# Optimization experiments

Hardware: AMD Instinct MI355X
Metric: run time of the kernel (lower is better)

## Reference

```python
import jax, jax.numpy as jnp
import numpy as np

N_NODES = 100000
N_EDGES = 3200000
IN_CH = 256
OUT_CH = 1


def setup_inputs() -> dict:
    key = jax.random.key(0)
    ks = jax.random.split(key, 8)
    x = jax.random.normal(ks[0], (N_NODES, IN_CH), dtype=jnp.float32)
    edge_index = jax.random.randint(ks[1], (2, N_EDGES), 0, N_NODES, dtype=jnp.int64 if jax.config.jax_enable_x64 else jnp.int32)
    s_in = 1.0 / np.sqrt(IN_CH)
    Wq = jax.random.uniform(ks[2], (IN_CH, OUT_CH), jnp.float32, -s_in, s_in)
    bq = jax.random.uniform(ks[3], (OUT_CH,), jnp.float32, -s_in, s_in)
    Wk = jax.random.uniform(ks[4], (IN_CH, OUT_CH), jnp.float32, -s_in, s_in)
    bk = jax.random.uniform(ks[5], (OUT_CH,), jnp.float32, -s_in, s_in)
    Wv = jax.random.uniform(ks[6], (IN_CH, IN_CH), jnp.float32, -s_in, s_in)
    bv = jax.random.uniform(ks[7], (IN_CH,), jnp.float32, -s_in, s_in)
    return {"x": x, "edge_index": edge_index, "Wq": Wq, "bq": bq,
            "Wk": Wk, "bk": bk, "Wv": Wv, "bv": bv}


def reference(x, edge_index, Wq, bq, Wk, bk, Wv, bv):
    num_nodes = x.shape[0]
    q = x @ Wq + bq                       # [N, out_ch]
    k = x @ Wk + bk                       # [N, out_ch]
    v = x @ Wv + bv                       # [N, in_ch]
    row, col = edge_index[0], edge_index[1]
    # edge attention logits: gather + dot over out_ch
    att = jnp.sum(q[row] * k[col], axis=-1)          # [E]
    att = jax.nn.leaky_relu(att, negative_slope=0.2)
    att = jax.nn.softmax(att, axis=0)                # softmax over ALL edges (dim=0)
    # scatter-add edge attention to source nodes
    attention_weights = jax.ops.segment_sum(att, row, num_segments=num_nodes)  # [N]
    graph_emb = jnp.sum(attention_weights[:, None] * v, axis=0)                # [in_ch]
    return graph_emb, attention_weights
```

## Files before the change

kernel.cpp:

```cpp
#include <hip/hip_runtime.h>

#define N_NODES 100000
#define N_EDGES 3200000
#define CH 256

#define EPB_S 8192
#define GS 391
#define NB2 25
#define BSZ 4096
#define G_AGG 10
#define SLICE 40
#define GRID_QK 1563
#define GRID_POOL 512
#define YCOPY 16

#define OFF_TOTAL  0
#define OFF_PTOT   16
#define OFF_YU16   528
#define OFF_PRE    4624
#define OFF_Q      14800
#define OFF_K      114800
#define OFF_AWU    214800
#define OFF_PART   314800
#define OFF_EX     1338800
#define OFF_ROW    4541872

__global__ __launch_bounds__(256) void k_qk(const float* __restrict__ x,
                                            const float* __restrict__ Wq,
                                            const float* __restrict__ bq,
                                            const float* __restrict__ Wk,
                                            const float* __restrict__ bk,
                                            float* __restrict__ q,
                                            float* __restrict__ k,
                                            float* __restrict__ yu16) {
    int t = threadIdx.x;
    if (blockIdx.x < 16) yu16[blockIdx.x * 256 + t] = 0.0f;
    int w = t >> 6, lane = t & 63;
    int g = lane >> 4, seg = lane & 15;
    float4 wq4[4], wk4[4];
    #pragma unroll
    for (int j = 0; j < 4; ++j) {
        wq4[j] = ((const float4*)Wq)[seg + 16 * j];
        wk4[j] = ((const float4*)Wk)[seg + 16 * j];
    }
    float bqs = bq[0], bks = bk[0];
    int base = blockIdx.x * 64 + w * 16 + g;
    #pragma unroll
    for (int i = 0; i < 4; ++i) {
        int n = base + i * 4;
        if (n < N_NODES) {
            const float4* xr = (const float4*)(x + (size_t)n * CH);
            float dq = 0.0f, dk = 0.0f;
            #pragma unroll
            for (int j = 0; j < 4; ++j) {
                float4 xv = xr[seg + 16 * j];
                dq = fmaf(xv.x, wq4[j].x, fmaf(xv.y, wq4[j].y,
                     fmaf(xv.z, wq4[j].z, fmaf(xv.w, wq4[j].w, dq))));
                dk = fmaf(xv.x, wk4[j].x, fmaf(xv.y, wk4[j].y,
                     fmaf(xv.z, wk4[j].z, fmaf(xv.w, wk4[j].w, dk))));
            }
            dq += __shfl_down(dq, 8); dq += __shfl_down(dq, 4);
            dq += __shfl_down(dq, 2); dq += __shfl_down(dq, 1);
            dk += __shfl_down(dk, 8); dk += __shfl_down(dk, 4);
            dk += __shfl_down(dk, 2); dk += __shfl_down(dk, 1);
            if (seg == 0) { q[n] = dq + bqs; k[n] = dk + bks; }
        }
    }
}

__global__ __launch_bounds__(512) void k_sort(const int* __restrict__ ei,
                                              const float* __restrict__ q,
                                              const float* __restrict__ k,
                                              float* __restrict__ ex_out,
                                              unsigned short* __restrict__ row_out,
                                              int* __restrict__ pre) {
    __shared__ int cnt[8][NB2];
    __shared__ int base8[8][NB2];
    __shared__ int pref[NB2 + 1];
    __shared__ int bsum[NB2];
    __shared__ float lex[EPB_S];
    __shared__ unsigned short lrow[EPB_S];
    int t = threadIdx.x, blk = blockIdx.x, w = t >> 6;
    int e0 = blk * EPB_S;
    int ecnt = min(EPB_S, N_EDGES - e0);
    for (int i = t; i < 8 * NB2; i += 512) ((int*)cnt)[i] = 0;
    __syncthreads();
    int rr[16]; float ee[16];
    #pragma unroll
    for (int j = 0; j < 16; ++j) {
        int i = j * 512 + t;
        if (i < ecnt) {
            int r = ei[e0 + i], c = ei[N_EDGES + e0 + i];
            float v = q[r] * k[c];
            v = (v >= 0.0f) ? v : 0.2f * v;
            rr[j] = r; ee[j] = __expf(v);
            atomicAdd(&cnt[w][r >> 12], 1);
        } else rr[j] = -1;
    }
    __syncthreads();
    if (t < NB2) {
        int s = 0;
        #pragma unroll
        for (int ww = 0; ww < 8; ++ww) { base8[ww][t] = s; s += cnt[ww][t]; }
        bsum[t] = s;
    }
    __syncthreads();
    if (t == 0) {
        int run = 0;
        #pragma unroll
        for (int b = 0; b < NB2; ++b) { pref[b] = run; run += bsum[b]; }
        pref[NB2] = run;
    }
    __syncthreads();
    if (t < 8 * NB2) {
        int ww = t / NB2, b = t - ww * NB2;
        base8[ww][b] += pref[b];
    }
    if (t < NB2 + 1) pre[blk * 26 + t] = pref[t];
    __syncthreads();
    #pragma unroll
    for (int j = 0; j < 16; ++j) {
        if (rr[j] >= 0) {
            int b = rr[j] >> 12;
            int p = atomicAdd(&base8[w][b], 1);
            lex[p] = ee[j];
            lrow[p] = (unsigned short)(rr[j] & (BSZ - 1));
        }
    }
    __syncthreads();
    size_t gb = (size_t)blk * EPB_S;
    for (int i = t; i < ecnt; i += 512) ex_out[gb + i] = lex[i];
    unsigned* ro = (unsigned*)(row_out + gb);
    const unsigned* lr = (const unsigned*)lrow;
    int words = (ecnt + 1) >> 1;
    for (int i = t; i < words; i += 512) ro[i] = lr[i];
}

__global__ __launch_bounds__(512) void k_agg(const float* __restrict__ ex,
                                             const unsigned short* __restrict__ row,
                                             const int* __restrict__ pre,
                                             float* __restrict__ partial) {
    int b = blockIdx.x / G_AGG, g = blockIdx.x % G_AGG;
    __shared__ float acc[BSZ];
    int t = threadIdx.x, w = t >> 6, lane = t & 63;
    for (int i = t; i < BSZ; i += 512) acc[i] = 0.0f;
    __syncthreads();
    int sb0 = g * SLICE, sb1 = min(sb0 + SLICE, GS);
    for (int sb = sb0 + w; sb < sb1; sb += 8) {
        size_t gbase = (size_t)sb * EPB_S;
        int s0 = pre[sb * 26 + b], s1 = pre[sb * 26 + b + 1];
        for (int i = s0 + lane; i < s1; i += 64)
            atomicAdd(&acc[row[gbase + i]], ex[gbase + i]);
    }
    __syncthreads();
    float* dst = partial + ((size_t)b * G_AGG + g) * BSZ;
    for (int i = t; i < BSZ; i += 512) dst[i] = acc[i];
}

__global__ __launch_bounds__(256) void k_fold(const float* __restrict__ partial,
                                              float* __restrict__ awu,
                                              float* __restrict__ ptot) {
    int t = threadIdx.x;
    int n = blockIdx.x * 256 + t;
    float s = 0.0f;
    if (n < N_NODES) {
        int b = n >> 12, off = n & (BSZ - 1);
        const float* p = partial + (size_t)b * G_AGG * BSZ + off;
        #pragma unroll
        for (int g = 0; g < G_AGG; ++g) s += p[(size_t)g * BSZ];
        awu[n] = s;
    }
    float r = s;
    #pragma unroll
    for (int off = 32; off; off >>= 1) r += __shfl_down(r, off);
    __shared__ float sm[4];
    if ((t & 63) == 0) sm[t >> 6] = r;
    __syncthreads();
    if (t == 0) ptot[blockIdx.x] = sm[0] + sm[1] + sm[2] + sm[3];
}

__global__ __launch_bounds__(256) void k_pool(const float* __restrict__ x,
                                              const float* __restrict__ awu,
                                              const float* __restrict__ ptot,
                                              float* __restrict__ totalp,
                                              float* __restrict__ yu16,
                                              float* __restrict__ aw_out) {
    int t = threadIdx.x, s = t >> 6, g = t & 63;
    float ts = ptot[t] + ((t + 256 < GS) ? ptot[t + 256] : 0.0f);
    #pragma unroll
    for (int off = 32; off; off >>= 1) ts += __shfl_down(ts, off);
    __shared__ float sm[4];
    __shared__ float tot;
    if (g == 0) sm[s] = ts;
    __syncthreads();
    if (t == 0) {
        tot = sm[0] + sm[1] + sm[2] + sm[3];
        if (blockIdx.x == 0) totalp[0] = tot;
    }
    __syncthreads();
    float inv = 1.0f / tot;

    const float4* X4 = (const float4*)x;
    float4 acc = make_float4(0.f, 0.f, 0.f, 0.f);
    for (int base = blockIdx.x * 8; base < N_NODES; base += GRID_POOL * 8) {
        float a0 = awu[base + s];
        float a1 = awu[base + 4 + s];
        float4 x0 = X4[(size_t)(base + s) * 64 + g];
        float4 x1 = X4[(size_t)(base + 4 + s) * 64 + g];
        acc.x = fmaf(a0, x0.x, acc.x); acc.y = fmaf(a0, x0.y, acc.y);
        acc.z = fmaf(a0, x0.z, acc.z); acc.w = fmaf(a0, x0.w, acc.w);
        acc.x = fmaf(a1, x1.x, acc.x); acc.y = fmaf(a1, x1.y, acc.y);
        acc.z = fmaf(a1, x1.z, acc.z); acc.w = fmaf(a1, x1.w, acc.w);
    }
    __shared__ float4 tmp4[4][64];
    tmp4[s][g] = acc;
    __syncthreads();
    const float* tmp = (const float*)tmp4;
    float sum = tmp[0 * 256 + t] + tmp[1 * 256 + t] + tmp[2 * 256 + t] + tmp[3 * 256 + t];
    atomicAdd(&yu16[(blockIdx.x & (YCOPY - 1)) * 256 + t], sum);
    for (int i = blockIdx.x * 256 + t; i < N_NODES; i += GRID_POOL * 256)
        aw_out[i] = awu[i] * inv;
}

__global__ __launch_bounds__(256) void k_final(const float* __restrict__ yu16,
                                               const float* __restrict__ totalp,
                                               const float* __restrict__ Wv,
                                               const float* __restrict__ bv,
                                               float* __restrict__ out) {
    __shared__ float ysh[256];
    __shared__ float red[256];
    int t = threadIdx.x;
    float inv = 1.0f / totalp[0];
    float yv = 0.0f;
    #pragma unroll
    for (int j = 0; j < YCOPY; ++j) yv += yu16[j * 256 + t];
    ysh[t] = yv * inv;
    __syncthreads();
    int c = blockIdx.x * 32 + (t & 31), rg = t >> 5;
    float acc = 0.0f;
    #pragma unroll
    for (int j = 0; j < 32; ++j) {
        int kk = rg * 32 + j;
        acc = fmaf(ysh[kk], Wv[(size_t)kk * CH + c], acc);
    }
    red[t] = acc;
    __syncthreads();
    if (t < 32) {
        float sv = 0.0f;
        #pragma unroll
        for (int j = 0; j < 8; ++j) sv += red[j * 32 + t];
        out[blockIdx.x * 32 + t] = sv + bv[blockIdx.x * 32 + t];
    }
}

extern "C" void kernel_launch(void* const* d_in, const int* in_sizes, int n_in,
                              void* d_out, int out_size, void* d_ws, size_t ws_size,
                              hipStream_t stream) {
    const float* x  = (const float*)d_in[0];
    const int*   ei = (const int*)d_in[1];
    const float* Wq = (const float*)d_in[2];
    const float* bq = (const float*)d_in[3];
    const float* Wk = (const float*)d_in[4];
    const float* bk = (const float*)d_in[5];
    const float* Wv = (const float*)d_in[6];
    const float* bv = (const float*)d_in[7];
    float* out = (float*)d_out;
    float* ws  = (float*)d_ws;

    float*          totalp  = ws + OFF_TOTAL;
    float*          ptot    = ws + OFF_PTOT;
    float*          yu16    = ws + OFF_YU16;
    int*            pre     = (int*)(ws + OFF_PRE);
    float*          q       = ws + OFF_Q;
    float*          k       = ws + OFF_K;
    float*          awu     = ws + OFF_AWU;
    float*          partial = ws + OFF_PART;
    float*          ex      = ws + OFF_EX;
    unsigned short* row     = (unsigned short*)(ws + OFF_ROW);

    hipLaunchKernelGGL(k_qk, dim3(GRID_QK), dim3(256), 0, stream,
                       x, Wq, bq, Wk, bk, q, k, yu16);
    hipLaunchKernelGGL(k_sort, dim3(GS), dim3(512), 0, stream,
                       ei, q, k, ex, row, pre);
    hipLaunchKernelGGL(k_agg, dim3(NB2 * G_AGG), dim3(512), 0, stream,
                       ex, row, pre, partial);
    hipLaunchKernelGGL(k_fold, dim3((N_NODES + 255) / 256), dim3(256), 0, stream,
                       partial, awu, ptot);
    hipLaunchKernelGGL(k_pool, dim3(GRID_POOL), dim3(256), 0, stream,
                       x, awu, ptot, totalp, yu16, out + CH);
    hipLaunchKernelGGL(k_final, dim3(8), dim3(256), 0, stream,
                       yu16, totalp, Wv, bv, out);
}
```

Measured before the change: 269.6 us.

## Remove fold kernel: fold partials in pool, per-block exp sums, smaller sort blocks

Drops the separate k_fold kernel. Each sort block now computes its own partial sum of exp values, and k_pool sums the G_AGG partial slices on the fly while pooling x. Sort blocks shrink from 8192 to 2048 edges with 256 threads, and aggregation is split into 16 groups instead of 10. The global atomic accumulation into 16 copies is replaced by per-block pooled outputs, which k_final reduces over all 512 rows. This saves one launch and the awu round trip, but adds a barrier per iteration in k_pool and a longer reduction in k_final.

```diff
diff --git a/kernel.cpp b/kernel.cpp
--- a/kernel.cpp
+++ b/kernel.cpp
@@ -4,26 +4,24 @@
 #define N_EDGES 3200000
 #define CH 256
 
-#define EPB_S 8192
-#define GS 391
+#define EPB 2048
+#define GS 1563
 #define NB2 25
 #define BSZ 4096
-#define G_AGG 10
-#define SLICE 40
+#define G_AGG 16
+#define SLICE 98
 #define GRID_QK 1563
 #define GRID_POOL 512
-#define YCOPY 16
 
 #define OFF_TOTAL  0
 #define OFF_PTOT   16
-#define OFF_YU16   528
-#define OFF_PRE    4624
-#define OFF_Q      14800
-#define OFF_K      114800
-#define OFF_AWU    214800
-#define OFF_PART   314800
-#define OFF_EX     1338800
-#define OFF_ROW    4541872
+#define OFF_YUP    1584
+#define OFF_PRE    132656
+#define OFF_Q      173296
+#define OFF_K      273296
+#define OFF_PART   373296
+#define OFF_EX     2011696
+#define OFF_ROW    5212720
 
 __global__ __launch_bounds__(256) void k_qk(const float* __restrict__ x,
                                             const float* __restrict__ Wq,
@@ -31,10 +29,8 @@
                                             const float* __restrict__ Wk,
                                             const float* __restrict__ bk,
                                             float* __restrict__ q,
-                                            float* __restrict__ k,
-                                            float* __restrict__ yu16) {
+                                            float* __restrict__ k) {
     int t = threadIdx.x;
-    if (blockIdx.x < 16) yu16[blockIdx.x * 256 + t] = 0.0f;
     int w = t >> 6, lane = t & 63;
     int g = lane >> 4, seg = lane & 15;
     float4 wq4[4], wk4[4];
@@ -68,41 +64,41 @@
     }
 }
 
-__global__ __launch_bounds__(512) void k_sort(const int* __restrict__ ei,
+__global__ __launch_bounds__(256) void k_sort(const int* __restrict__ ei,
                                               const float* __restrict__ q,
                                               const float* __restrict__ k,
                                               float* __restrict__ ex_out,
                                               unsigned short* __restrict__ row_out,
-                                              int* __restrict__ pre) {
-    __shared__ int cnt[8][NB2];
-    __shared__ int base8[8][NB2];
+                                              int* __restrict__ pre,
+                                              float* __restrict__ ptot) {
+    __shared__ int cnt[4][NB2];
+    __shared__ int bsum[NB2];
     __shared__ int pref[NB2 + 1];
-    __shared__ int bsum[NB2];
-    __shared__ float lex[EPB_S];
-    __shared__ unsigned short lrow[EPB_S];
+    __shared__ float lex[EPB];
+    __shared__ unsigned short lrow[EPB];
+    __shared__ float sm[4];
     int t = threadIdx.x, blk = blockIdx.x, w = t >> 6;
-    int e0 = blk * EPB_S;
-    int ecnt = min(EPB_S, N_EDGES - e0);
-    for (int i = t; i < 8 * NB2; i += 512) ((int*)cnt)[i] = 0;
-    __syncthreads();
-    int rr[16]; float ee[16];
-    #pragma unroll
-    for (int j = 0; j < 16; ++j) {
-        int i = j * 512 + t;
+    int e0 = blk * EPB;
+    int ecnt = min(EPB, N_EDGES - e0);
+    if (t < 4 * NB2) ((int*)cnt)[t] = 0;
+    __syncthreads();
+    int rr[8]; float ee[8];
+    #pragma unroll
+    for (int j = 0; j < 8; ++j) {
+        int i = j * 256 + t;
         if (i < ecnt) {
             int r = ei[e0 + i], c = ei[N_EDGES + e0 + i];
             float v = q[r] * k[c];
             v = (v >= 0.0f) ? v : 0.2f * v;
             rr[j] = r; ee[j] = __expf(v);
             atomicAdd(&cnt[w][r >> 12], 1);
-        } else rr[j] = -1;
+        } else { rr[j] = -1; ee[j] = 0.0f; }
     }
     __syncthreads();
     if (t < NB2) {
-        int s = 0;
-        #pragma unroll
-        for (int ww = 0; ww < 8; ++ww) { base8[ww][t] = s; s += cnt[ww][t]; }
-        bsum[t] = s;
+        int c0 = cnt[0][t], c1 = cnt[1][t], c2 = cnt[2][t], c3 = cnt[3][t];
+        cnt[0][t] = 0; cnt[1][t] = c0; cnt[2][t] = c0 + c1; cnt[3][t] = c0 + c1 + c2;
+        bsum[t] = c0 + c1 + c2 + c3;
     }
     __syncthreads();
     if (t == 0) {
@@ -112,99 +108,95 @@
         pref[NB2] = run;
     }
     __syncthreads();
-    if (t < 8 * NB2) {
-        int ww = t / NB2, b = t - ww * NB2;
-        base8[ww][b] += pref[b];
-    }
+    if (t < 4 * NB2) { int ww = t / NB2, b = t - ww * NB2; cnt[ww][b] += pref[b]; }
     if (t < NB2 + 1) pre[blk * 26 + t] = pref[t];
     __syncthreads();
     #pragma unroll
-    for (int j = 0; j < 16; ++j) {
+    for (int j = 0; j < 8; ++j) {
         if (rr[j] >= 0) {
             int b = rr[j] >> 12;
-            int p = atomicAdd(&base8[w][b], 1);
+            int p = atomicAdd(&cnt[w][b], 1);
             lex[p] = ee[j];
             lrow[p] = (unsigned short)(rr[j] & (BSZ - 1));
         }
     }
-    __syncthreads();
-    size_t gb = (size_t)blk * EPB_S;
-    for (int i = t; i < ecnt; i += 512) ex_out[gb + i] = lex[i];
+    float s = ((ee[0] + ee[1]) + (ee[2] + ee[3])) + ((ee[4] + ee[5]) + (ee[6] + ee[7]));
+    #pragma unroll
+    for (int off = 32; off; off >>= 1) s += __shfl_down(s, off);
+    if ((t & 63) == 0) sm[w] = s;
+    __syncthreads();
+    if (t == 0) ptot[blk] = sm[0] + sm[1] + sm[2] + sm[3];
+    size_t gb = (size_t)blk * EPB;
+    for (int i = t; i < ecnt; i += 256) ex_out[gb + i] = lex[i];
     unsigned* ro = (unsigned*)(row_out + gb);
     const unsigned* lr = (const unsigned*)lrow;
     int words = (ecnt + 1) >> 1;
-    for (int i = t; i < words; i += 512) ro[i] = lr[i];
-}
-
-__global__ __launch_bounds__(512) void k_agg(const float* __restrict__ ex,
+    for (int i = t; i < words; i += 256) ro[i] = lr[i];
+}
+
+__global__ __launch_bounds__(256) void k_agg(const float* __restrict__ ex,
                                              const unsigned short* __restrict__ row,
                                              const int* __restrict__ pre,
                                              float* __restrict__ partial) {
     int b = blockIdx.x / G_AGG, g = blockIdx.x % G_AGG;
     __shared__ float acc[BSZ];
     int t = threadIdx.x, w = t >> 6, lane = t & 63;
-    for (int i = t; i < BSZ; i += 512) acc[i] = 0.0f;
+    for (int i = t; i < BSZ; i += 256) acc[i] = 0.0f;
     __syncthreads();
     int sb0 = g * SLICE, sb1 = min(sb0 + SLICE, GS);
-    for (int sb = sb0 + w; sb < sb1; sb += 8) {
-        size_t gbase = (size_t)sb * EPB_S;
+    for (int sb = sb0 + w; sb < sb1; sb += 4) {
+        size_t gbase = (size_t)sb * EPB;
         int s0 = pre[sb * 26 + b], s1 = pre[sb * 26 + b + 1];
         for (int i = s0 + lane; i < s1; i += 64)
             atomicAdd(&acc[row[gbase + i]], ex[gbase + i]);
     }
     __syncthreads();
     float* dst = partial + ((size_t)b * G_AGG + g) * BSZ;
-    for (int i = t; i < BSZ; i += 512) dst[i] = acc[i];
-}
-
-__global__ __launch_bounds__(256) void k_fold(const float* __restrict__ partial,
-                                              float* __restrict__ awu,
-                                              float* __restrict__ ptot) {
-    int t = threadIdx.x;
-    int n = blockIdx.x * 256 + t;
-    float s = 0.0f;
-    if (n < N_NODES) {
-        int b = n >> 12, off = n & (BSZ - 1);
-        const float* p = partial + (size_t)b * G_AGG * BSZ + off;
-        #pragma unroll
-        for (int g = 0; g < G_AGG; ++g) s += p[(size_t)g * BSZ];
-        awu[n] = s;
-    }
-    float r = s;
-    #pragma unroll
-    for (int off = 32; off; off >>= 1) r += __shfl_down(r, off);
-    __shared__ float sm[4];
-    if ((t & 63) == 0) sm[t >> 6] = r;
-    __syncthreads();
-    if (t == 0) ptot[blockIdx.x] = sm[0] + sm[1] + sm[2] + sm[3];
+    for (int i = t; i < BSZ; i += 256) dst[i] = acc[i];
 }
 
 __global__ __launch_bounds__(256) void k_pool(const float* __restrict__ x,
-                                              const float* __restrict__ awu,
+                                              const float* __restrict__ partial,
                                               const float* __restrict__ ptot,
                                               float* __restrict__ totalp,
-                                              float* __restrict__ yu16,
+                                              float* __restrict__ yup,
                                               float* __restrict__ aw_out) {
     int t = threadIdx.x, s = t >> 6, g = t & 63;
-    float ts = ptot[t] + ((t + 256 < GS) ? ptot[t + 256] : 0.0f);
+    float ts = 0.0f;
+    for (int i = t; i < GS; i += 256) ts += ptot[i];
     #pragma unroll
     for (int off = 32; off; off >>= 1) ts += __shfl_down(ts, off);
     __shared__ float sm[4];
-    __shared__ float tot;
+    __shared__ float totsh;
     if (g == 0) sm[s] = ts;
     __syncthreads();
     if (t == 0) {
-        tot = sm[0] + sm[1] + sm[2] + sm[3];
-        if (blockIdx.x == 0) totalp[0] = tot;
-    }
-    __syncthreads();
-    float inv = 1.0f / tot;
-
+        totsh = sm[0] + sm[1] + sm[2] + sm[3];
+        if (blockIdx.x == 0) totalp[0] = totsh;
+    }
+    __syncthreads();
+    float inv = 1.0f / totsh;
+
+    __shared__ float awA[2][8], awB[2][8];
     const float4* X4 = (const float4*)x;
     float4 acc = make_float4(0.f, 0.f, 0.f, 0.f);
-    for (int base = blockIdx.x * 8; base < N_NODES; base += GRID_POOL * 8) {
-        float a0 = awu[base + s];
-        float a1 = awu[base + 4 + s];
+    int p = 0;
+    for (int base = blockIdx.x * 8; base < N_NODES; base += GRID_POOL * 8, p ^= 1) {
+        int bkt = base >> 12, off = base & (BSZ - 1);
+        float pv = 0.0f;
+        if (t < 128) {
+            int sl = t >> 3, no = t & 7;
+            pv = partial[((size_t)bkt * G_AGG + sl) * BSZ + off + no];
+        }
+        pv += __shfl_down(pv, 32);
+        pv += __shfl_down(pv, 16);
+        pv += __shfl_down(pv, 8);
+        if (t < 8) awA[p][t] = pv;
+        else if (t >= 64 && t < 72) awB[p][t - 64] = pv;
+        __syncthreads();
+        float a0 = awA[p][s] + awB[p][s];
+        float a1 = awA[p][4 + s] + awB[p][4 + s];
+        if (t < 8) aw_out[base + t] = (awA[p][t] + awB[p][t]) * inv;
         float4 x0 = X4[(size_t)(base + s) * 64 + g];
         float4 x1 = X4[(size_t)(base + 4 + s) * 64 + g];
         acc.x = fmaf(a0, x0.x, acc.x); acc.y = fmaf(a0, x0.y, acc.y);
@@ -212,17 +204,16 @@
         acc.x = fmaf(a1, x1.x, acc.x); acc.y = fmaf(a1, x1.y, acc.y);
         acc.z = fmaf(a1, x1.z, acc.z); acc.w = fmaf(a1, x1.w, acc.w);
     }
+    __syncthreads();
     __shared__ float4 tmp4[4][64];
     tmp4[s][g] = acc;
     __syncthreads();
     const float* tmp = (const float*)tmp4;
     float sum = tmp[0 * 256 + t] + tmp[1 * 256 + t] + tmp[2 * 256 + t] + tmp[3 * 256 + t];
-    atomicAdd(&yu16[(blockIdx.x & (YCOPY - 1)) * 256 + t], sum);
-    for (int i = blockIdx.x * 256 + t; i < N_NODES; i += GRID_POOL * 256)
-        aw_out[i] = awu[i] * inv;
-}
-
-__global__ __launch_bounds__(256) void k_final(const float* __restrict__ yu16,
+    yup[(size_t)blockIdx.x * 256 + t] = sum;
+}
+
+__global__ __launch_bounds__(256) void k_final(const float* __restrict__ yup,
                                                const float* __restrict__ totalp,
                                                const float* __restrict__ Wv,
                                                const float* __restrict__ bv,
@@ -232,8 +223,8 @@
     int t = threadIdx.x;
     float inv = 1.0f / totalp[0];
     float yv = 0.0f;
-    #pragma unroll
-    for (int j = 0; j < YCOPY; ++j) yv += yu16[j * 256 + t];
+    #pragma unroll 8
+    for (int r = 0; r < GRID_POOL; ++r) yv += yup[(size_t)r * 256 + t];
     ysh[t] = yv * inv;
     __syncthreads();
     int c = blockIdx.x * 32 + (t & 31), rg = t >> 5;
@@ -269,25 +260,22 @@
 
     float*          totalp  = ws + OFF_TOTAL;
     float*          ptot    = ws + OFF_PTOT;
-    float*          yu16    = ws + OFF_YU16;
+    float*          yup     = ws + OFF_YUP;
     int*            pre     = (int*)(ws + OFF_PRE);
     float*          q       = ws + OFF_Q;
     float*          k       = ws + OFF_K;
-    float*          awu     = ws + OFF_AWU;
     float*          partial = ws + OFF_PART;
     float*          ex      = ws + OFF_EX;
     unsigned short* row     = (unsigned short*)(ws + OFF_ROW);
 
     hipLaunchKernelGGL(k_qk, dim3(GRID_QK), dim3(256), 0, stream,
-                       x, Wq, bq, Wk, bk, q, k, yu16);
-    hipLaunchKernelGGL(k_sort, dim3(GS), dim3(512), 0, stream,
-                       ei, q, k, ex, row, pre);
-    hipLaunchKernelGGL(k_agg, dim3(NB2 * G_AGG), dim3(512), 0, stream,
+                       x, Wq, bq, Wk, bk, q, k);
+    hipLaunchKernelGGL(k_sort, dim3(GS), dim3(256), 0, stream,
+                       ei, q, k, ex, row, pre, ptot);
+    hipLaunchKernelGGL(k_agg, dim3(NB2 * G_AGG), dim3(256), 0, stream,
                        ex, row, pre, partial);
-    hipLaunchKernelGGL(k_fold, dim3((N_NODES + 255) / 256), dim3(256), 0, stream,
-                       partial, awu, ptot);
     hipLaunchKernelGGL(k_pool, dim3(GRID_POOL), dim3(256), 0, stream,
-                       x, awu, ptot, totalp, yu16, out + CH);
+                       x, partial, ptot, totalp, yup, out + CH);
     hipLaunchKernelGGL(k_final, dim3(8), dim3(256), 0, stream,
-                       yu16, totalp, Wv, bv, out);
-}
+                       yup, totalp, Wv, bv, out);
+}
```

Result: slower. 295.5 us (+9.6%).
